# Performance work log

Hardware: AMD Instinct MI355X
Metric: run time of the kernel (lower is better)

Reference implementation:

```python
import jax, jax.numpy as jnp
import numpy as np

EPS_NORM = 1e-12  # torch F.normalize eps


def _resize_bilinear_ac(x, H, W):
    # Bilinear resize with align_corners=True on NCHW tensor x.
    h, w = x.shape[-2], x.shape[-1]
    ys = jnp.linspace(0.0, h - 1.0, H)
    xs = jnp.linspace(0.0, w - 1.0, W)
    y0 = jnp.floor(ys).astype(jnp.int32); y1 = jnp.minimum(y0 + 1, h - 1)
    x0 = jnp.floor(xs).astype(jnp.int32); x1 = jnp.minimum(x0 + 1, w - 1)
    wy = (ys - y0).astype(x.dtype)[None, None, :, None]
    wx = (xs - x0).astype(x.dtype)
    rows = x[:, :, y0, :] * (1 - wy) + x[:, :, y1, :] * wy  # (B,C,H,w)
    return rows[:, :, :, x0] * (1 - wx) + rows[:, :, :, x1] * wx  # (B,C,H,W)


def _icc(p, b):
    # p: (b, 19, hw) row-stochastic over hw.
    # M[i, j] = KLDiv(input=p_i, target=p_j, batchmean) = (1/b) * sum p_j*(log p_j - p_i)
    # NOTE: original code passes probabilities (not log-probs) as KLDiv input; kept faithful.
    E = jnp.sum(p * jnp.log(p), axis=(0, 2))            # (19,) sum_b,k p log p
    G = jnp.einsum('bik,bjk->ij', p, p)                  # (19,19) sum_b,k p_i p_j
    M = (E[None, :] - G) / b
    sym = jnp.triu(M) + jnp.triu(M, 1).T                 # loop writes value for i<=j to both [i,j],[j,i]
    nrm = jnp.maximum(jnp.linalg.norm(sym, axis=1, keepdims=True), EPS_NORM)
    return sym / nrm                                     # F.normalize(dim=1)


def reference(s_out, t_out, t_logit, s_logit, conv_w, conv_b):
    T = 1.0  # temperature
    # --- pi_loss ---
    B, C, H, W = t_out.shape
    s1 = _resize_bilinear_ac(s_out, H, W)
    s1 = jnp.einsum('bchw,oc->bohw', s1, conv_w[:, :, 0, 0]) + conv_b[None, :, None, None]
    log_ps = jax.nn.log_softmax(s1 / T, axis=1)
    pt = jax.nn.softmax(t_out / T, axis=1)
    # torch KLDivLoss() default reduction='mean' (mean over ALL elements)
    pi_loss = jnp.mean(pt * (jnp.log(pt) - log_ps))
    # --- lo_loss ---
    b, n, h, w = s_logit.shape
    tl = _resize_bilinear_ac(t_logit, h, w)
    s = jax.nn.softmax(s_logit.reshape(b, n, h * w) / T, axis=2)
    t = jax.nn.softmax(tl.reshape(b, n, h * w) / T, axis=2)
    ICCS = _icc(s, b)
    ICCT = _icc(t, b)
    lo_loss = jnp.sum((ICCS - ICCT) ** 2)
    return pi_loss, lo_loss


def setup_inputs() -> dict:
    key = jax.random.key(0)
    k = jax.random.split(key, 6)
    return {
        's_out': jax.random.normal(k[0], (8, 128, 33, 33), jnp.float32),
        't_out': jax.random.normal(k[1], (8, 768, 65, 65), jnp.float32),
        't_logit': jax.random.normal(k[2], (8, 19, 65, 65), jnp.float32),
        's_logit': jax.random.normal(k[3], (8, 19, 129, 129), jnp.float32),
        'conv_w': jax.random.normal(k[4], (768, 128, 1, 1), jnp.float32) * 0.05,
        'conv_b': jax.random.normal(k[5], (768,), jnp.float32) * 0.05,
    }
```

## Files before the change

### kernel.cpp

```cpp
#include <hip/hip_runtime.h>
#include <math.h>

#define WS_E0   0
#define WS_E1   19
#define WS_G0   64
#define WS_G1   448
#define WS_Z    1152
#define WS_WBF  2048
#define WS_PART 51200

typedef __bf16 bf16x8 __attribute__((ext_vector_type(8)));
typedef float  f32x4  __attribute__((ext_vector_type(4)));
typedef const __attribute__((address_space(1))) unsigned int guint;
typedef       __attribute__((address_space(3))) unsigned int luint;

__global__ void k_init(const float* __restrict__ conv_w, float* __restrict__ ws,
                       float* __restrict__ out) {
    const int bx = blockIdx.x, tid = threadIdx.x;
    if (bx < 96) {
        __bf16* Wb = (__bf16*)(ws + WS_WBF);
        #pragma unroll
        for (int j = 0; j < 4; j++) {
            int idx = bx * 1024 + j * 256 + tid;
            Wb[idx] = (__bf16)conv_w[idx];
        }
    } else {
        for (int k = tid; k < 2048; k += 256) ws[k] = 0.f;
        if (tid < 2) out[tid] = 0.f;
    }
}

__device__ __forceinline__ float t_resized(const float* __restrict__ Trow, int k) {
    int y = k / 129, x = k - y * 129;
    int y0 = y >> 1, x0 = x >> 1;
    int y1 = y0 + (y & 1), x1 = x0 + (x & 1);
    float fy = 0.5f * (float)(y & 1), fx = 0.5f * (float)(x & 1);
    float v00 = Trow[y0 * 65 + x0], v01 = Trow[y0 * 65 + x1];
    float v10 = Trow[y1 * 65 + x0], v11 = Trow[y1 * 65 + x1];
    float r0 = v00 + fx * (v01 - v00);
    float r1 = v10 + fx * (v11 - v10);
    return r0 + fy * (r1 - r0);
}

__launch_bounds__(256, 3)
__global__ void k_main(const float* __restrict__ s_out, const float* __restrict__ t_out,
                       const float* __restrict__ conv_w, const float* __restrict__ bias,
                       const float* __restrict__ s_logit, const float* __restrict__ t_logit,
                       float* __restrict__ ws, float* __restrict__ out) {
    __shared__ __align__(16) char lds[50176];
    const int tid = threadIdx.x;
    const int bx  = blockIdx.x;

    if (bx >= 304 && bx < 2416) {
        const int idx     = bx - 304;
        const int quarter = idx & 3;
        const int bs      = idx >> 2;
        const int b       = bs / 66;
        const int strip   = bs - b * 66;
        const int px0     = strip * 64;

        const int l = tid & 63, g = tid >> 6, q = l >> 4, n = l & 15;
        const int og = quarter * 192 + g * 16;

        const float* base_t = t_out + (size_t)(b * 768 + og) * 4225;
        int off[4];
        #pragma unroll
        for (int j = 0; j < 4; j++) {
            int col = ((n * 4) + j * 16) & 63;
            off[j] = (j * 4 + q) * 4225 + px0 + col;
        }
        int colr[4];
        #pragma unroll
        for (int pt = 0; pt < 4; pt++)
            colr[pt] = (((pt * 16 + (n & 12) - q * 16) & 63)) + (n & 3);

        auto issue_t = [&](int cc) {
            char* lb = (cc == 2) ? (lds + g * 4096) : (lds + 17408 + cc * 16384 + g * 4096);
            const float* gb = base_t + (size_t)cc * 64 * 4225;
            #pragma unroll
            for (int j = 0; j < 4; j++)
                __builtin_amdgcn_global_load_lds((guint*)(gb + off[j]),
                                                 (luint*)(lb + j * 1024), 16, 0, 0);
        };

        issue_t(0);
        issue_t(1);

        __bf16* xs = (__bf16*)lds;

        {
            const float* Sb = s_out + b * 128 * 1089;
            #pragma unroll
            for (int ii = 0; ii < 32; ii++) {
                int id2 = tid + ii * 256;
                int c = id2 >> 6, px = id2 & 63;
                int hw = px0 + px;
                int h = hw / 65, w = hw - h * 65;
                int y0 = h >> 1, x0 = w >> 1;
                int y1 = y0 + (h & 1), x1 = x0 + (w & 1);
                float wy = 0.5f * (float)(h & 1), wx = 0.5f * (float)(w & 1);
                const float* Sc = Sb + c * 1089;
                float v00 = Sc[y0 * 33 + x0], v01 = Sc[y0 * 33 + x1];
                float v10 = Sc[y1 * 33 + x0], v11 = Sc[y1 * 33 + x1];
                float r0 = v00 + wx * (v01 - v00);
                float r1 = v10 + wx * (v11 - v10);
                xs[px * 136 + c] = (__bf16)(r0 + wy * (r1 - r0));
            }
        }
        asm volatile("s_waitcnt lgkmcnt(0)" ::: "memory");
        __builtin_amdgcn_s_barrier();
        __builtin_amdgcn_sched_barrier(0);

        bf16x8 bfrag[4][4];
        #pragma unroll
        for (int pt = 0; pt < 4; pt++)
            #pragma unroll
            for (int kf = 0; kf < 4; kf++)
                bfrag[pt][kf] = *(const bf16x8*)&xs[(pt * 16 + n) * 136 + kf * 32 + q * 8];

        const __bf16* Wbf = (const __bf16*)(ws + WS_WBF);
        bf16x8 afr[3][4];
        f32x4  bq[3];
        auto load_a = [&](int cc) {
            const __bf16* Wr = Wbf + (size_t)(og + cc * 64 + n) * 128 + q * 8;
            #pragma unroll
            for (int kf = 0; kf < 4; kf++) afr[cc][kf] = *(const bf16x8*)(Wr + kf * 32);
            bq[cc] = *(const f32x4*)&bias[og + cc * 64 + q * 4];
        };
        load_a(0);
        load_a(1);

        asm volatile("s_waitcnt lgkmcnt(0)" ::: "memory");
        __builtin_amdgcn_s_barrier();
        __builtin_amdgcn_sched_barrier(0);
        issue_t(2);

        float Zt[4], St[4], Dd[4], Zs[4];
        #pragma unroll
        for (int pt = 0; pt < 4; pt++) { Zt[pt] = 0.f; St[pt] = 0.f; Dd[pt] = 0.f; Zs[pt] = 0.f; }

        #pragma unroll
        for (int c = 0; c < 3; c++) {
            if (c == 0)      asm volatile("s_waitcnt vmcnt(8)" ::: "memory");
            else if (c == 1) asm volatile("s_waitcnt vmcnt(4)" ::: "memory");
            else             asm volatile("s_waitcnt vmcnt(0)" ::: "memory");
            if (c == 1) load_a(2);

            const float* tw = (const float*)((c == 2) ? (lds + g * 4096)
                                                      : (lds + 17408 + c * 16384 + g * 4096));
            #pragma unroll
            for (int pt = 0; pt < 4; pt++) {
                f32x4 a0 = {0.f, 0.f, 0.f, 0.f};
                #pragma unroll
                for (int kf = 0; kf < 4; kf++)
                    a0 = __builtin_amdgcn_mfma_f32_16x16x32_bf16(afr[c][kf], bfrag[pt][kf], a0, 0, 0, 0);
                #pragma unroll
                for (int r = 0; r < 4; r++) {
                    float tv  = tw[(q * 4 + r) * 64 + colr[pt]];
                    float s1v = a0[r] + bq[c][r];
                    float e   = __expf(tv);
                    Zt[pt] += e;
                    St[pt]  = fmaf(e, tv,  St[pt]);
                    Dd[pt]  = fmaf(e, s1v, Dd[pt]);
                    Zs[pt] += __expf(s1v);
                }
            }
        }

        __syncthreads();
        float* scr = (float*)lds;
        {
            int p = g * 4 + q;
            #pragma unroll
            for (int pt = 0; pt < 4; pt++) {
                f32x4 v = {Zt[pt], St[pt], Dd[pt], Zs[pt]};
                *(f32x4*)&scr[(pt * 16 + n) * 68 + p * 4] = v;
            }
        }
        __syncthreads();
        if (tid < 64) {
            float Z = 0.f, S = 0.f, D = 0.f, Z2 = 0.f;
            #pragma unroll
            for (int p = 0; p < 16; p++) {
                f32x4 v = *(const f32x4*)&scr[tid * 68 + p * 4];
                Z += v[0]; S += v[1]; D += v[2]; Z2 += v[3];
            }
            f32x4 o4 = {Z, S, D, Z2};
            *(f32x4*)&ws[WS_PART + (((size_t)quarter * 8 + b) * 4224 + px0 + tid) * 4] = o4;
        }
    } else if (bx < 304) {
        float* red = (float*)lds;
        int row  = bx;
        int side = (row >= 152) ? 1 : 0;
        int r    = side ? row - 152 : row;
        const float* src = side ? (t_logit + r * 4225) : (s_logit + r * 16641);

        float z = 0.f, s = 0.f;
        #pragma unroll 4
        for (int k = tid; k < 16641; k += 256) {
            float v = side ? t_resized(src, k) : src[k];
            float e = __expf(v);
            z += e;
            s = fmaf(e, v, s);
        }
        for (int off = 32; off > 0; off >>= 1) { z += __shfl_down(z, off); s += __shfl_down(s, off); }
        if ((tid & 63) == 0) { red[tid >> 6] = z; red[4 + (tid >> 6)] = s; }
        __syncthreads();
        if (tid == 0) {
            float Z = red[0] + red[1] + red[2] + red[3];
            float S = red[4] + red[5] + red[6] + red[7];
            ws[WS_Z + row] = Z;
            atomicAdd(&ws[(side ? WS_E1 : WS_E0) + (r % 19)], S / Z - logf(Z));
        }
    } else {
        float* xc  = (float*)lds;
        float* red = (float*)lds + 128;
        const int b = bx - 2416;
        if (tid < 128) xc[tid] = s_out[((size_t)b * 128 + tid) * 1089 + 1088];
        __syncthreads();
        float z = 0.f, s = 0.f, d = 0.f, z2 = 0.f;
        #pragma unroll
        for (int rep = 0; rep < 3; rep++) {
            int o = tid + rep * 256;
            const float* Wr = conv_w + (size_t)o * 128;
            float s1 = bias[o];
            for (int cc = 0; cc < 128; cc++) s1 = fmaf(Wr[cc], xc[cc], s1);
            float tv = t_out[((size_t)(b * 768 + o)) * 4225 + 4224];
            float e  = __expf(tv);
            z += e; s = fmaf(e, tv, s); d = fmaf(e, s1, d); z2 += __expf(s1);
        }
        for (int off = 32; off > 0; off >>= 1) {
            z += __shfl_down(z, off); s += __shfl_down(s, off);
            d += __shfl_down(d, off); z2 += __shfl_down(z2, off);
        }
        if ((tid & 63) == 0) {
            int wv = tid >> 6;
            red[wv] = z; red[4 + wv] = s; red[8 + wv] = d; red[12 + wv] = z2;
        }
        __syncthreads();
        if (tid == 0) {
            float Z = red[0] + red[1] + red[2] + red[3];
            float S = red[4] + red[5] + red[6] + red[7];
            float D = red[8] + red[9] + red[10] + red[11];
            float Z2 = red[12] + red[13] + red[14] + red[15];
            float contrib = (S - D) / Z - logf(Z) + logf(Z2);
            atomicAdd(out, contrib * (1.0f / 25958400.0f));
        }
    }
}

#define KT 512
#define KP 516
__global__ void k_mid(const float* __restrict__ s_logit, const float* __restrict__ t_logit,
                      float* __restrict__ ws, float* __restrict__ out) {
    __shared__ __align__(16) char lds[39296];
    const int tid = threadIdx.x;
    const int bx  = blockIdx.x;

    if (bx < 528) {
        float* pbuf  = (float*)lds;
        float* rowiz = (float*)(lds + 39216);
        int side = (bx >= 264) ? 1 : 0;
        int rm   = side ? bx - 264 : bx;
        int b = rm / 33, kt = rm - b * 33;
        int k0 = kt * KT;

        if (tid < 19) rowiz[tid] = 1.0f / ws[WS_Z + side * 152 + b * 19 + tid];
        __syncthreads();

        for (int i = 0; i < 19; i++) {
            const float* src = side ? (t_logit + (b * 19 + i) * 4225) : (s_logit + (b * 19 + i) * 16641);
            float iz = rowiz[i];
            #pragma unroll
            for (int kl = tid; kl < KT; kl += 256) {
                int k = k0 + kl;
                float p = 0.f;
                if (k < 16641) {
                    float v = side ? t_resized(src, k) : src[k];
                    p = __expf(v) * iz;
                }
                pbuf[i * KP + kl] = p;
            }
        }
        __syncthreads();

        if (tid < 190) {
            int t = tid, i = 0;
            while (t >= 19 - i) { t -= 19 - i; i++; }
            int j = i + t;
            const float* pi_ = &pbuf[i * KP];
            const float* pj_ = &pbuf[j * KP];
            float g0 = 0.f, g1 = 0.f, g2 = 0.f, g3 = 0.f;
            #pragma unroll 2
            for (int kl = 0; kl < KT; kl += 16) {
                float4 a0 = *(const float4*)&pi_[kl];      float4 c0 = *(const float4*)&pj_[kl];
                float4 a1 = *(const float4*)&pi_[kl + 4];  float4 c1 = *(const float4*)&pj_[kl + 4];
                float4 a2 = *(const float4*)&pi_[kl + 8];  float4 c2 = *(const float4*)&pj_[kl + 8];
                float4 a3 = *(const float4*)&pi_[kl + 12]; float4 c3 = *(const float4*)&pj_[kl + 12];
                g0 = fmaf(a0.x, c0.x, g0); g0 = fmaf(a0.y, c0.y, g0);
                g0 = fmaf(a0.z, c0.z, g0); g0 = fmaf(a0.w, c0.w, g0);
                g1 = fmaf(a1.x, c1.x, g1); g1 = fmaf(a1.y, c1.y, g1);
                g1 = fmaf(a1.z, c1.z, g1); g1 = fmaf(a1.w, c1.w, g1);
                g2 = fmaf(a2.x, c2.x, g2); g2 = fmaf(a2.y, c2.y, g2);
                g2 = fmaf(a2.z, c2.z, g2); g2 = fmaf(a2.w, c2.w, g2);
                g3 = fmaf(a3.x, c3.x, g3); g3 = fmaf(a3.y, c3.y, g3);
                g3 = fmaf(a3.z, c3.z, g3); g3 = fmaf(a3.w, c3.w, g3);
            }
            atomicAdd(&ws[(side ? WS_G1 : WS_G0) + i * 19 + j], (g0 + g1) + (g2 + g3));
        }
    } else {
        float* red = (float*)lds;
        int gp = (bx - 528) * 256 + tid;
        int b  = gp / 4224;
        int tp = gp - b * 4224;
        float Z = 0.f, S = 0.f, D = 0.f, Z2 = 0.f;
        #pragma unroll
        for (int qq = 0; qq < 4; qq++) {
            f32x4 v = *(const f32x4*)&ws[WS_PART + (((size_t)qq * 8 + b) * 4224 + tp) * 4];
            Z += v[0]; S += v[1]; D += v[2]; Z2 += v[3];
        }
        float contrib = (S - D) / Z - logf(Z) + logf(Z2);
        for (int off = 32; off > 0; off >>= 1) contrib += __shfl_down(contrib, off);
        if ((tid & 63) == 0) red[tid >> 6] = contrib;
        __syncthreads();
        if (tid == 0)
            atomicAdd(out, (red[0] + red[1] + red[2] + red[3]) * (1.0f / 25958400.0f));
    }
}

__global__ void k_final(const float* __restrict__ ws, float* __restrict__ out) {
    __shared__ float Ms[361], Mt[361], ns[19], nt[19];
    __shared__ float red[8];
    int tid = threadIdx.x;
    if (tid < 361) {
        int i = tid / 19, j = tid - i * 19;
        int lo = min(i, j), hi = max(i, j);
        Ms[tid] = (ws[WS_E0 + hi] - ws[WS_G0 + lo * 19 + hi]) * 0.125f;
        Mt[tid] = (ws[WS_E1 + hi] - ws[WS_G1 + lo * 19 + hi]) * 0.125f;
    }
    __syncthreads();
    if (tid < 19) {
        float as = 0.f, at = 0.f;
        for (int j = 0; j < 19; j++) {
            as = fmaf(Ms[tid * 19 + j], Ms[tid * 19 + j], as);
            at = fmaf(Mt[tid * 19 + j], Mt[tid * 19 + j], at);
        }
        ns[tid] = fmaxf(sqrtf(as), 1e-12f);
        nt[tid] = fmaxf(sqrtf(at), 1e-12f);
    }
    __syncthreads();
    float d = 0.f;
    if (tid < 361) {
        int i = tid / 19;
        float v = Ms[tid] / ns[i] - Mt[tid] / nt[i];
        d = v * v;
    }
    for (int off = 32; off > 0; off >>= 1) d += __shfl_down(d, off);
    if ((tid & 63) == 0) red[tid >> 6] = d;
    __syncthreads();
    if (tid == 0) out[1] = red[0] + red[1] + red[2] + red[3] + red[4] + red[5];
}

extern "C" void kernel_launch(void* const* d_in, const int* in_sizes, int n_in,
                              void* d_out, int out_size, void* d_ws, size_t ws_size,
                              hipStream_t stream) {
    const float* s_out   = (const float*)d_in[0];
    const float* t_out   = (const float*)d_in[1];
    const float* t_logit = (const float*)d_in[2];
    const float* s_logit = (const float*)d_in[3];
    const float* conv_w  = (const float*)d_in[4];
    const float* conv_b  = (const float*)d_in[5];
    float* out = (float*)d_out;
    float* ws  = (float*)d_ws;

    k_init<<<dim3(97), dim3(256), 0, stream>>>(conv_w, ws, out);
    k_main<<<dim3(2424), dim3(256), 0, stream>>>(s_out, t_out, conv_w, conv_b,
                                                 s_logit, t_logit, ws, out);
    k_mid<<<dim3(660), dim3(256), 0, stream>>>(s_logit, t_logit, ws, out);
    k_final<<<dim3(1), dim3(384), 0, stream>>>(ws, out);
}
```

Before: 239.7 us.

## Process all output channels per block with triple-buffered streaming, drop partial buffer

Each main-pass block now covers all 768 output channels for its pixel strip instead of one quarter. It streams twelve channel chunks through a three-slot LDS ring, with weight and t_out prefetch issued inside the loop. Because the softmax sums are complete inside the block, the per-pixel KL term is finished there and added straight to the output. This removes the workspace partial buffer and the combine blocks in the middle kernel. The trade is 4x fewer main blocks, 528 instead of 2112, plus longer per-block serial chains, which may leave the GPU under-occupied.

```diff
diff --git a/kernel.cpp b/kernel.cpp
--- a/kernel.cpp
+++ b/kernel.cpp
@@ -7,7 +7,6 @@
 #define WS_G1   448
 #define WS_Z    1152
 #define WS_WBF  2048
-#define WS_PART 51200
 
 typedef __bf16 bf16x8 __attribute__((ext_vector_type(8)));
 typedef float  f32x4  __attribute__((ext_vector_type(4)));
@@ -51,16 +50,14 @@
     const int tid = threadIdx.x;
     const int bx  = blockIdx.x;
 
-    if (bx >= 304 && bx < 2416) {
-        const int idx     = bx - 304;
-        const int quarter = idx & 3;
-        const int bs      = idx >> 2;
-        const int b       = bs / 66;
-        const int strip   = bs - b * 66;
-        const int px0     = strip * 64;
+    if (bx >= 304 && bx < 832) {
+        const int idx   = bx - 304;
+        const int b     = idx / 66;
+        const int strip = idx - b * 66;
+        const int px0   = strip * 64;
 
         const int l = tid & 63, g = tid >> 6, q = l >> 4, n = l & 15;
-        const int og = quarter * 192 + g * 16;
+        const int og = g * 16;
 
         const float* base_t = t_out + (size_t)(b * 768 + og) * 4225;
         int off[4];
@@ -75,7 +72,8 @@
             colr[pt] = (((pt * 16 + (n & 12) - q * 16) & 63)) + (n & 3);
 
         auto issue_t = [&](int cc) {
-            char* lb = (cc == 2) ? (lds + g * 4096) : (lds + 17408 + cc * 16384 + g * 4096);
+            int k = cc % 3;
+            char* lb = (k == 2 ? lds : lds + 17408 + k * 16384) + g * 4096;
             const float* gb = base_t + (size_t)cc * 64 * 4225;
             #pragma unroll
             for (int j = 0; j < 4; j++)
@@ -122,10 +120,12 @@
         bf16x8 afr[3][4];
         f32x4  bq[3];
         auto load_a = [&](int cc) {
-            const __bf16* Wr = Wbf + (size_t)(og + cc * 64 + n) * 128 + q * 8;
-            #pragma unroll
-            for (int kf = 0; kf < 4; kf++) afr[cc][kf] = *(const bf16x8*)(Wr + kf * 32);
-            bq[cc] = *(const f32x4*)&bias[og + cc * 64 + q * 4];
+            int s = cc % 3;
+            int row0 = cc * 64 + og;
+            const __bf16* Wr = Wbf + (size_t)(row0 + n) * 128 + q * 8;
+            #pragma unroll
+            for (int kf = 0; kf < 4; kf++) afr[s][kf] = *(const bf16x8*)(Wr + kf * 32);
+            bq[s] = *(const f32x4*)&bias[row0 + q * 4];
         };
         load_a(0);
         load_a(1);
@@ -140,24 +140,23 @@
         for (int pt = 0; pt < 4; pt++) { Zt[pt] = 0.f; St[pt] = 0.f; Dd[pt] = 0.f; Zs[pt] = 0.f; }
 
         #pragma unroll
-        for (int c = 0; c < 3; c++) {
-            if (c == 0)      asm volatile("s_waitcnt vmcnt(8)" ::: "memory");
-            else if (c == 1) asm volatile("s_waitcnt vmcnt(4)" ::: "memory");
-            else             asm volatile("s_waitcnt vmcnt(0)" ::: "memory");
-            if (c == 1) load_a(2);
-
-            const float* tw = (const float*)((c == 2) ? (lds + g * 4096)
-                                                      : (lds + 17408 + c * 16384 + g * 4096));
+        for (int c = 0; c < 12; c++) {
+            if (c == 0 || c == 10) asm volatile("s_waitcnt vmcnt(9)"  ::: "memory");
+            else if (c == 11)      asm volatile("s_waitcnt vmcnt(0)"  ::: "memory");
+            else                   asm volatile("s_waitcnt vmcnt(13)" ::: "memory");
+
+            const int k = c % 3;
+            const float* tw = (const float*)((k == 2 ? lds : lds + 17408 + k * 16384) + g * 4096);
             #pragma unroll
             for (int pt = 0; pt < 4; pt++) {
                 f32x4 a0 = {0.f, 0.f, 0.f, 0.f};
                 #pragma unroll
                 for (int kf = 0; kf < 4; kf++)
-                    a0 = __builtin_amdgcn_mfma_f32_16x16x32_bf16(afr[c][kf], bfrag[pt][kf], a0, 0, 0, 0);
+                    a0 = __builtin_amdgcn_mfma_f32_16x16x32_bf16(afr[k][kf], bfrag[pt][kf], a0, 0, 0, 0);
                 #pragma unroll
                 for (int r = 0; r < 4; r++) {
                     float tv  = tw[(q * 4 + r) * 64 + colr[pt]];
-                    float s1v = a0[r] + bq[c][r];
+                    float s1v = a0[r] + bq[k][r];
                     float e   = __expf(tv);
                     Zt[pt] += e;
                     St[pt]  = fmaf(e, tv,  St[pt]);
@@ -165,6 +164,8 @@
                     Zs[pt] += __expf(s1v);
                 }
             }
+            if (c <= 9) load_a(c + 2);
+            if (c <= 8) issue_t(c + 3);
         }
 
         __syncthreads();
@@ -185,8 +186,10 @@
                 f32x4 v = *(const f32x4*)&scr[tid * 68 + p * 4];
                 Z += v[0]; S += v[1]; D += v[2]; Z2 += v[3];
             }
-            f32x4 o4 = {Z, S, D, Z2};
-            *(f32x4*)&ws[WS_PART + (((size_t)quarter * 8 + b) * 4224 + px0 + tid) * 4] = o4;
+            float contrib = (S - D) / Z - logf(Z) + logf(Z2);
+            #pragma unroll
+            for (int o = 32; o > 0; o >>= 1) contrib += __shfl_down(contrib, o);
+            if (tid == 0) atomicAdd(out, contrib * (1.0f / 25958400.0f));
         }
     } else if (bx < 304) {
         float* red = (float*)lds;
@@ -215,7 +218,7 @@
     } else {
         float* xc  = (float*)lds;
         float* red = (float*)lds + 128;
-        const int b = bx - 2416;
+        const int b = bx - 832;
         if (tid < 128) xc[tid] = s_out[((size_t)b * 128 + tid) * 1089 + 1088];
         __syncthreads();
         float z = 0.f, s = 0.f, d = 0.f, z2 = 0.f;
@@ -257,74 +260,56 @@
     const int tid = threadIdx.x;
     const int bx  = blockIdx.x;
 
-    if (bx < 528) {
-        float* pbuf  = (float*)lds;
-        float* rowiz = (float*)(lds + 39216);
-        int side = (bx >= 264) ? 1 : 0;
-        int rm   = side ? bx - 264 : bx;
-        int b = rm / 33, kt = rm - b * 33;
-        int k0 = kt * KT;
-
-        if (tid < 19) rowiz[tid] = 1.0f / ws[WS_Z + side * 152 + b * 19 + tid];
-        __syncthreads();
-
-        for (int i = 0; i < 19; i++) {
-            const float* src = side ? (t_logit + (b * 19 + i) * 4225) : (s_logit + (b * 19 + i) * 16641);
-            float iz = rowiz[i];
-            #pragma unroll
-            for (int kl = tid; kl < KT; kl += 256) {
-                int k = k0 + kl;
-                float p = 0.f;
-                if (k < 16641) {
-                    float v = side ? t_resized(src, k) : src[k];
-                    p = __expf(v) * iz;
-                }
-                pbuf[i * KP + kl] = p;
-            }
-        }
-        __syncthreads();
-
-        if (tid < 190) {
-            int t = tid, i = 0;
-            while (t >= 19 - i) { t -= 19 - i; i++; }
-            int j = i + t;
-            const float* pi_ = &pbuf[i * KP];
-            const float* pj_ = &pbuf[j * KP];
-            float g0 = 0.f, g1 = 0.f, g2 = 0.f, g3 = 0.f;
-            #pragma unroll 2
-            for (int kl = 0; kl < KT; kl += 16) {
-                float4 a0 = *(const float4*)&pi_[kl];      float4 c0 = *(const float4*)&pj_[kl];
-                float4 a1 = *(const float4*)&pi_[kl + 4];  float4 c1 = *(const float4*)&pj_[kl + 4];
-                float4 a2 = *(const float4*)&pi_[kl + 8];  float4 c2 = *(const float4*)&pj_[kl + 8];
-                float4 a3 = *(const float4*)&pi_[kl + 12]; float4 c3 = *(const float4*)&pj_[kl + 12];
-                g0 = fmaf(a0.x, c0.x, g0); g0 = fmaf(a0.y, c0.y, g0);
-                g0 = fmaf(a0.z, c0.z, g0); g0 = fmaf(a0.w, c0.w, g0);
-                g1 = fmaf(a1.x, c1.x, g1); g1 = fmaf(a1.y, c1.y, g1);
-                g1 = fmaf(a1.z, c1.z, g1); g1 = fmaf(a1.w, c1.w, g1);
-                g2 = fmaf(a2.x, c2.x, g2); g2 = fmaf(a2.y, c2.y, g2);
-                g2 = fmaf(a2.z, c2.z, g2); g2 = fmaf(a2.w, c2.w, g2);
-                g3 = fmaf(a3.x, c3.x, g3); g3 = fmaf(a3.y, c3.y, g3);
-                g3 = fmaf(a3.z, c3.z, g3); g3 = fmaf(a3.w, c3.w, g3);
-            }
-            atomicAdd(&ws[(side ? WS_G1 : WS_G0) + i * 19 + j], (g0 + g1) + (g2 + g3));
-        }
-    } else {
-        float* red = (float*)lds;
-        int gp = (bx - 528) * 256 + tid;
-        int b  = gp / 4224;
-        int tp = gp - b * 4224;
-        float Z = 0.f, S = 0.f, D = 0.f, Z2 = 0.f;
-        #pragma unroll
-        for (int qq = 0; qq < 4; qq++) {
-            f32x4 v = *(const f32x4*)&ws[WS_PART + (((size_t)qq * 8 + b) * 4224 + tp) * 4];
-            Z += v[0]; S += v[1]; D += v[2]; Z2 += v[3];
-        }
-        float contrib = (S - D) / Z - logf(Z) + logf(Z2);
-        for (int off = 32; off > 0; off >>= 1) contrib += __shfl_down(contrib, off);
-        if ((tid & 63) == 0) red[tid >> 6] = contrib;
-        __syncthreads();
-        if (tid == 0)
-            atomicAdd(out, (red[0] + red[1] + red[2] + red[3]) * (1.0f / 25958400.0f));
+    float* pbuf  = (float*)lds;
+    float* rowiz = (float*)(lds + 39216);
+    int side = (bx >= 264) ? 1 : 0;
+    int rm   = side ? bx - 264 : bx;
+    int b = rm / 33, kt = rm - b * 33;
+    int k0 = kt * KT;
+
+    if (tid < 19) rowiz[tid] = 1.0f / ws[WS_Z + side * 152 + b * 19 + tid];
+    __syncthreads();
+
+    for (int i = 0; i < 19; i++) {
+        const float* src = side ? (t_logit + (size_t)(b * 19 + i) * 4225)
+                                : (s_logit + (size_t)(b * 19 + i) * 16641);
+        float iz = rowiz[i];
+        #pragma unroll
+        for (int kl = tid; kl < KT; kl += 256) {
+            int k = k0 + kl;
+            float p = 0.f;
+            if (k < 16641) {
+                float v = side ? t_resized(src, k) : src[k];
+                p = __expf(v) * iz;
+            }
+            pbuf[i * KP + kl] = p;
+        }
+    }
+    __syncthreads();
+
+    if (tid < 190) {
+        int t = tid, i = 0;
+        while (t >= 19 - i) { t -= 19 - i; i++; }
+        int j = i + t;
+        const float* pi_ = &pbuf[i * KP];
+        const float* pj_ = &pbuf[j * KP];
+        float g0 = 0.f, g1 = 0.f, g2 = 0.f, g3 = 0.f;
+        #pragma unroll 2
+        for (int kl = 0; kl < KT; kl += 16) {
+            float4 a0 = *(const float4*)&pi_[kl];      float4 c0 = *(const float4*)&pj_[kl];
+            float4 a1 = *(const float4*)&pi_[kl + 4];  float4 c1 = *(const float4*)&pj_[kl + 4];
+            float4 a2 = *(const float4*)&pi_[kl + 8];  float4 c2 = *(const float4*)&pj_[kl + 8];
+            float4 a3 = *(const float4*)&pi_[kl + 12]; float4 c3 = *(const float4*)&pj_[kl + 12];
+            g0 = fmaf(a0.x, c0.x, g0); g0 = fmaf(a0.y, c0.y, g0);
+            g0 = fmaf(a0.z, c0.z, g0); g0 = fmaf(a0.w, c0.w, g0);
+            g1 = fmaf(a1.x, c1.x, g1); g1 = fmaf(a1.y, c1.y, g1);
+            g1 = fmaf(a1.z, c1.z, g1); g1 = fmaf(a1.w, c1.w, g1);
+            g2 = fmaf(a2.x, c2.x, g2); g2 = fmaf(a2.y, c2.y, g2);
+            g2 = fmaf(a2.z, c2.z, g2); g2 = fmaf(a2.w, c2.w, g2);
+            g3 = fmaf(a3.x, c3.x, g3); g3 = fmaf(a3.y, c3.y, g3);
+            g3 = fmaf(a3.z, c3.z, g3); g3 = fmaf(a3.w, c3.w, g3);
+        }
+        atomicAdd(&ws[(side ? WS_G1 : WS_G0) + i * 19 + j], (g0 + g1) + (g2 + g3));
     }
 }
 
@@ -374,8 +359,8 @@
     float* ws  = (float*)d_ws;
 
     k_init<<<dim3(97), dim3(256), 0, stream>>>(conv_w, ws, out);
-    k_main<<<dim3(2424), dim3(256), 0, stream>>>(s_out, t_out, conv_w, conv_b,
-                                                 s_logit, t_logit, ws, out);
-    k_mid<<<dim3(660), dim3(256), 0, stream>>>(s_logit, t_logit, ws, out);
+    k_main<<<dim3(840), dim3(256), 0, stream>>>(s_out, t_out, conv_w, conv_b,
+                                                s_logit, t_logit, ws, out);
+    k_mid<<<dim3(528), dim3(256), 0, stream>>>(s_logit, t_logit, ws, out);
     k_final<<<dim3(1), dim3(384), 0, stream>>>(ws, out);
 }
```

After: 277.3 us. 1.16x slower.
